# Optimization experiments

Measured on AMD Instinct MI355X. Metric: run time of the kernel, lower is better.

## Reference

```python
import jax, jax.numpy as jnp
import numpy as np

N = 131072  # time steps
D = 4       # SDE state dimension


def setup_inputs() -> dict:
    key = jax.random.key(0)
    k = jax.random.split(key, 6)
    F = 0.1 * jax.random.normal(k[0], (D, D), jnp.float32)  # only shape/dtype used by filter
    H = jnp.zeros((1, D), jnp.float32).at[0, 0].set(1.0)    # observe first state component
    P_inf = jnp.eye(D, dtype=jnp.float32)
    # stable per-step transitions: spectral radius ~0.9
    A_seq = 0.9 * jnp.eye(D, dtype=jnp.float32)[None] + 0.02 * jax.random.normal(k[1], (N, D, D), jnp.float32)
    # PSD process noise per step
    S = 0.05 * jax.random.normal(k[2], (N, D, D), jnp.float32)
    Q_seq = jnp.einsum('nij,nkj->nik', S, S) + 1e-3 * jnp.eye(D, dtype=jnp.float32)[None]
    residual = jax.random.normal(k[3], (N,), jnp.float32)   # y - mean_fn(times)
    mask = jnp.ones((N,), jnp.float32)                      # all steps observed
    R_seq = 0.1 + 0.05 * jax.random.uniform(k[4], (N,), jnp.float32)  # noise_var + floor
    return dict(F=F, H=H, P_inf=P_inf, A_seq=A_seq, Q_seq=Q_seq,
                residual=residual, mask=mask, R_seq=R_seq)


def _kalman_filter(F, H, P_inf, A_seq, Q_seq, residual, mask, R_seq):
    d = F.shape[0]
    eye = jnp.eye(d, dtype=F.dtype)
    h = H[0]  # (d,)
    log_2pi = jnp.log(2.0 * jnp.pi).astype(F.dtype)

    def step(carry, inputs):
        m, P = carry
        A, Q, r_n, mask_n, R_n = inputs
        m_pred = A @ m
        P_pred = A @ P @ A.T + Q
        P_pred = 0.5 * (P_pred + P_pred.T)
        Ph = P_pred @ h                 # (d,)
        S = h @ Ph + R_n                # innovation variance
        innov = r_n - h @ m_pred
        is_obs = mask_n == 1
        S_safe = jnp.where(is_obs, S, 1.0)
        K = jnp.where(is_obs, Ph / S_safe, jnp.zeros_like(Ph))
        m_new = m_pred + K * innov
        I_KH = eye - K[:, None] * h[None, :]
        P_new = I_KH @ P_pred @ I_KH.T + R_n * (K[:, None] * K[None, :])
        P_new = 0.5 * (P_new + P_new.T)
        ll = jnp.where(is_obs, -0.5 * (log_2pi + jnp.log(S_safe) + innov * innov / S_safe), 0.0)
        return (m_new, P_new), (m_pred, P_pred, m_new, P_new, ll)

    m0 = jnp.zeros(d, dtype=F.dtype)
    _, (m_pred_seq, P_pred_seq, m_filt_seq, P_filt_seq, ll_seq) = jax.lax.scan(
        step, (m0, P_inf), (A_seq, Q_seq, residual, mask, R_seq))
    return m_pred_seq, P_pred_seq, m_filt_seq, P_filt_seq, jnp.sum(ll_seq)


def _rts_smoother(m_pred_seq, P_pred_seq, m_filt_seq, P_filt_seq, A_seq):
    def step(carry, inputs):
        m_ns, P_ns = carry
        m_f, P_f, m_pn, P_pn, A_n = inputs
        J = jnp.linalg.solve(P_pn.T, A_n @ P_f.T).T
        m_s = m_f + J @ (m_ns - m_pn)
        P_s = P_f + J @ (P_ns - P_pn) @ J.T
        P_s = 0.5 * (P_s + P_s.T)
        return (m_s, P_s), (m_s, P_s)

    m_T = m_filt_seq[-1]
    P_T = P_filt_seq[-1]
    inputs = (m_filt_seq[:-1], P_filt_seq[:-1], m_pred_seq[1:], P_pred_seq[1:], A_seq[1:])
    _, (m_s, P_s) = jax.lax.scan(step, (m_T, P_T), inputs, reverse=True)
    return (jnp.concatenate([m_s, m_T[None]], axis=0),
            jnp.concatenate([P_s, P_T[None]], axis=0))


def reference(F, H, P_inf, A_seq, Q_seq, residual, mask, R_seq):
    m_pred, P_pred, m_filt, P_filt, log_marginal = _kalman_filter(
        F, H, P_inf, A_seq, Q_seq, residual, mask, R_seq)
    m_smooth, P_smooth = _rts_smoother(m_pred, P_pred, m_filt, P_filt, A_seq)
    h = H[0]
    means = m_smooth @ h                                   # (N,) observation-space means
    vars_ = jnp.einsum('i,nij,j->n', h, P_smooth, h)       # (N,) marginal variances
    return means, vars_, log_marginal
```

## Files before the change

### kernel.cpp

```cpp
#include <hip/hip_runtime.h>
#include <math.h>

#define NN 131072
#define WUP 32
#define TPB 256
#define NBLK (NN / TPB)
#define WINF (TPB + WUP + 1)
#define WINB (TPB + WUP - 1)
#define LOG2PI 1.8378770664093453f

typedef __attribute__((ext_vector_type(2))) float f2;

__device__ float4 g_f[5][NN];
__device__ float4 g_J[4][NN];
__device__ float4 g_W0[NN];
__device__ float4 g_W1[NN];
__device__ float2 g_W2[NN];
__device__ float4 g_u[NN];
__device__ double g_llb[NBLK];

__device__ __forceinline__ f2 bc(float s) {
  f2 r = {s, s};
  return r;
}
#define PF(a, b, c) __builtin_elementwise_fma((a), (b), (c))

template <int E>
__device__ __forceinline__ void ldpk(const float4 (*s)[E], int w, f2* M) {
#pragma unroll
  for (int c = 0; c < 4; ++c) {
    float4 v = s[c][w];
    M[2 * c] = f2{v.x, v.y};
    M[2 * c + 1] = f2{v.z, v.w};
  }
}

__device__ __forceinline__ void sym_rows(const float4 t0, const float4 t1, const float2 t2,
                                         f2* M) {
  M[0] = f2{t0.x, t0.y};
  M[1] = f2{t0.z, t0.w};
  M[2] = f2{t0.y, t1.x};
  M[3] = f2{t1.y, t1.z};
  M[4] = f2{t0.z, t1.y};
  M[5] = f2{t1.w, t2.x};
  M[6] = f2{t0.w, t1.z};
  M[7] = f2{t2.x, t2.y};
}

__device__ __forceinline__ void kf_step_pk(const f2* __restrict__ AT, const f2* __restrict__ Q,
                                           float r, float mk, float R, f2* __restrict__ m,
                                           f2* __restrict__ P, float& Ss, float& innov,
                                           bool& obs) {
  float m0 = m[0][0], m1 = m[0][1], m2_ = m[1][0], m3 = m[1][1];
  f2 mp[2];
#pragma unroll
  for (int p = 0; p < 2; ++p) {
    f2 acc = AT[p] * bc(m0);
    acc = PF(bc(m1), AT[2 + p], acc);
    acc = PF(bc(m2_), AT[4 + p], acc);
    acc = PF(bc(m3), AT[6 + p], acc);
    mp[p] = acc;
  }

  f2 T[8];
#pragma unroll
  for (int i = 0; i < 4; ++i) {
    float a0 = AT[0 + (i >> 1)][i & 1];
    float a1 = AT[2 + (i >> 1)][i & 1];
    float a2 = AT[4 + (i >> 1)][i & 1];
    float a3 = AT[6 + (i >> 1)][i & 1];
#pragma unroll
    for (int p = 0; p < 2; ++p) {
      f2 acc = P[p] * bc(a0);
      acc = PF(bc(a1), P[2 + p], acc);
      acc = PF(bc(a2), P[4 + p], acc);
      acc = PF(bc(a3), P[6 + p], acc);
      T[2 * i + p] = acc;
    }
  }

  f2 Pp[8];
#pragma unroll
  for (int i = 0; i < 4; ++i) {
    float t0 = T[2 * i][0], t1 = T[2 * i][1], t2 = T[2 * i + 1][0], t3 = T[2 * i + 1][1];
#pragma unroll
    for (int p = 0; p < 2; ++p) {
      f2 acc = PF(bc(t0), AT[p], Q[2 * i + p]);
      acc = PF(bc(t1), AT[2 + p], acc);
      acc = PF(bc(t2), AT[4 + p], acc);
      acc = PF(bc(t3), AT[6 + p], acc);
      Pp[2 * i + p] = acc;
    }
  }

  float S = Pp[0][0] + R;
  innov = r - mp[0][0];
  obs = (mk == 1.0f);
  Ss = obs ? S : 1.0f;
  float kf = obs ? __builtin_amdgcn_rcpf(S) : 0.0f;
  f2 K[2] = {Pp[0] * bc(kf), Pp[1] * bc(kf)};
#pragma unroll
  for (int p = 0; p < 2; ++p) m[p] = PF(K[p], bc(innov), mp[p]);

#pragma unroll
  for (int i = 0; i < 4; ++i) {
    float Ki = K[i >> 1][i & 1];
#pragma unroll
    for (int p = 0; p < 2; ++p) P[2 * i + p] = PF(bc(-Ki), Pp[p], Pp[2 * i + p]);
  }
}

__device__ __forceinline__ void chol_solve_pk(const f2* __restrict__ S, const f2* __restrict__ T,
                                              f2* __restrict__ X) {
  float s00 = S[0][0];
  float s10 = S[2][0], s11 = S[2][1];
  float s20 = S[4][0], s21 = S[4][1], s22 = S[5][0];
  float s30 = S[6][0], s31 = S[6][1], s32 = S[7][0], s33 = S[7][1];
  float i00 = __builtin_amdgcn_rsqf(s00);
  float l10 = s10 * i00, l20 = s20 * i00, l30 = s30 * i00;
  float i11 = __builtin_amdgcn_rsqf(s11 - l10 * l10);
  float l21 = (s21 - l20 * l10) * i11;
  float l31 = (s31 - l30 * l10) * i11;
  float i22 = __builtin_amdgcn_rsqf(s22 - l20 * l20 - l21 * l21);
  float l32 = (s32 - l30 * l20 - l31 * l21) * i22;
  float i33 = __builtin_amdgcn_rsqf(s33 - l30 * l30 - l31 * l31 - l32 * l32);
#pragma unroll
  for (int c = 0; c < 4; ++c) {
    float t0 = T[0 + (c >> 1)][c & 1];
    float t1 = T[2 + (c >> 1)][c & 1];
    float t2 = T[4 + (c >> 1)][c & 1];
    float t3 = T[6 + (c >> 1)][c & 1];
    float y0 = t0 * i00;
    float y1 = (t1 - l10 * y0) * i11;
    float y2 = (t2 - l20 * y0 - l21 * y1) * i22;
    float y3 = (t3 - l30 * y0 - l31 * y1 - l32 * y2) * i33;
    float x3 = y3 * i33;
    float x2 = (y2 - l32 * x3) * i22;
    float x1 = (y1 - l21 * x2 - l31 * x3) * i11;
    float x0 = (y0 - l10 * x1 - l20 * x2 - l30 * x3) * i00;
    X[0 + (c >> 1)][c & 1] = x0;
    X[2 + (c >> 1)][c & 1] = x1;
    X[4 + (c >> 1)][c & 1] = x2;
    X[6 + (c >> 1)][c & 1] = x3;
  }
}

__device__ __forceinline__ void make_record_pk(int n, const f2* __restrict__ m,
                                               const f2* __restrict__ P,
                                               const f2* __restrict__ AT,
                                               const f2* __restrict__ Q) {
  float m0 = m[0][0], m1 = m[0][1], m2_ = m[1][0], m3 = m[1][1];
  f2 pm[2];
#pragma unroll
  for (int p = 0; p < 2; ++p) {
    f2 acc = AT[p] * bc(m0);
    acc = PF(bc(m1), AT[2 + p], acc);
    acc = PF(bc(m2_), AT[4 + p], acc);
    acc = PF(bc(m3), AT[6 + p], acc);
    pm[p] = acc;
  }

  f2 T[8];
#pragma unroll
  for (int i = 0; i < 4; ++i) {
    float a0 = AT[0 + (i >> 1)][i & 1];
    float a1 = AT[2 + (i >> 1)][i & 1];
    float a2 = AT[4 + (i >> 1)][i & 1];
    float a3 = AT[6 + (i >> 1)][i & 1];
#pragma unroll
    for (int p = 0; p < 2; ++p) {
      f2 acc = P[p] * bc(a0);
      acc = PF(bc(a1), P[2 + p], acc);
      acc = PF(bc(a2), P[4 + p], acc);
      acc = PF(bc(a3), P[6 + p], acc);
      T[2 * i + p] = acc;
    }
  }

  f2 Ppn[8];
#pragma unroll
  for (int i = 0; i < 4; ++i) {
    float t0 = T[2 * i][0], t1 = T[2 * i][1], t2 = T[2 * i + 1][0], t3 = T[2 * i + 1][1];
#pragma unroll
    for (int p = 0; p < 2; ++p) {
      f2 acc = PF(bc(t0), AT[p], Q[2 * i + p]);
      acc = PF(bc(t1), AT[2 + p], acc);
      acc = PF(bc(t2), AT[4 + p], acc);
      acc = PF(bc(t3), AT[6 + p], acc);
      Ppn[2 * i + p] = acc;
    }
  }

  f2 X[8];
  chol_solve_pk(Ppn, T, X);

  float p0 = pm[0][0], p1 = pm[0][1], p2 = pm[1][0], p3 = pm[1][1];
  f2 u[2];
#pragma unroll
  for (int p = 0; p < 2; ++p) {
    f2 acc = X[p] * bc(p0);
    acc = PF(bc(p1), X[2 + p], acc);
    acc = PF(bc(p2), X[4 + p], acc);
    acc = PF(bc(p3), X[6 + p], acc);
    u[p] = m[p] - acc;
  }

  f2 Jp[8];
#pragma unroll
  for (int i = 0; i < 4; ++i) {
    float x0 = X[0 + (i >> 1)][i & 1];
    float x1 = X[2 + (i >> 1)][i & 1];
    float x2 = X[4 + (i >> 1)][i & 1];
    float x3 = X[6 + (i >> 1)][i & 1];
#pragma unroll
    for (int p = 0; p < 2; ++p) {
      f2 acc = Ppn[p] * bc(x0);
      acc = PF(bc(x1), Ppn[2 + p], acc);
      acc = PF(bc(x2), Ppn[4 + p], acc);
      acc = PF(bc(x3), Ppn[6 + p], acc);
      Jp[2 * i + p] = acc;
    }
  }
  f2 W[8];
#pragma unroll
  for (int i = 0; i < 4; ++i) {
    float j0 = Jp[2 * i][0], j1 = Jp[2 * i][1], j2 = Jp[2 * i + 1][0], j3 = Jp[2 * i + 1][1];
#pragma unroll
    for (int p = 0; p < 2; ++p) {
      f2 acc = X[p] * bc(j0);
      acc = PF(bc(j1), X[2 + p], acc);
      acc = PF(bc(j2), X[4 + p], acc);
      acc = PF(bc(j3), X[6 + p], acc);
      W[2 * i + p] = P[2 * i + p] - acc;
    }
  }

#pragma unroll
  for (int i = 0; i < 4; ++i)
    g_J[i][n] = make_float4(X[2 * i][0], X[2 * i][1], X[2 * i + 1][0], X[2 * i + 1][1]);
  g_W0[n] = make_float4(W[0][0], W[0][1], W[1][0], W[1][1]);
  g_W1[n] = make_float4(W[2][1], W[3][0], W[3][1], W[5][0]);
  g_W2[n] = make_float2(W[5][1], W[7][1]);
  g_u[n] = make_float4(u[0][0], u[0][1], u[1][0], u[1][1]);
}

__device__ __forceinline__ void rts_affine_pk(const f2* __restrict__ X, const f2* __restrict__ W,
                                              const f2* __restrict__ u, f2* __restrict__ ms,
                                              f2* __restrict__ Ps) {
  float s0 = ms[0][0], s1 = ms[0][1], s2 = ms[1][0], s3 = ms[1][1];
  f2 nms[2];
#pragma unroll
  for (int p = 0; p < 2; ++p) {
    f2 acc = PF(bc(s0), X[p], u[p]);
    acc = PF(bc(s1), X[2 + p], acc);
    acc = PF(bc(s2), X[4 + p], acc);
    acc = PF(bc(s3), X[6 + p], acc);
    nms[p] = acc;
  }
  f2 V[8];
#pragma unroll
  for (int i = 0; i < 4; ++i) {
    float x0 = X[0 + (i >> 1)][i & 1];
    float x1 = X[2 + (i >> 1)][i & 1];
    float x2 = X[4 + (i >> 1)][i & 1];
    float x3 = X[6 + (i >> 1)][i & 1];
#pragma unroll
    for (int p = 0; p < 2; ++p) {
      f2 acc = Ps[p] * bc(x0);
      acc = PF(bc(x1), Ps[2 + p], acc);
      acc = PF(bc(x2), Ps[4 + p], acc);
      acc = PF(bc(x3), Ps[6 + p], acc);
      V[2 * i + p] = acc;
    }
  }
#pragma unroll
  for (int i = 0; i < 4; ++i) {
    float v0 = V[2 * i][0], v1 = V[2 * i][1], v2 = V[2 * i + 1][0], v3 = V[2 * i + 1][1];
#pragma unroll
    for (int p = 0; p < 2; ++p) {
      f2 acc = PF(bc(v0), X[p], W[2 * i + p]);
      acc = PF(bc(v1), X[2 + p], acc);
      acc = PF(bc(v2), X[4 + p], acc);
      acc = PF(bc(v3), X[6 + p], acc);
      Ps[2 * i + p] = acc;
    }
  }
  ms[0] = nms[0];
  ms[1] = nms[1];
}

__global__ __launch_bounds__(TPB, 1) void fwd_kernel(const float* __restrict__ P_inf,
                                                     const float* __restrict__ A_seq,
                                                     const float* __restrict__ Q_seq,
                                                     const float* __restrict__ residual,
                                                     const float* __restrict__ mask,
                                                     const float* __restrict__ R_seq) {
  __shared__ float4 sAT[4][WINF];
  __shared__ float4 sQ0[WINF], sQ1[WINF];
  __shared__ float2 sQ2[WINF];
  __shared__ float4 sRM[WINF];
  __shared__ double sh[TPB];

  const int B = blockIdx.x * TPB;
  const int base = B - WUP;
  const float4* Af4 = (const float4*)A_seq;
  const float4* Qf4 = (const float4*)Q_seq;
  for (int f = threadIdx.x; f < WINF * 4; f += TPB) {
    int w = f >> 2, c = f & 3;
    int k = base + w;
    k = k < 0 ? 0 : (k > NN - 1 ? NN - 1 : k);
    float4 rowA = Af4[(size_t)k * 4 + c];
    ((float*)&sAT[0][w])[c] = rowA.x;
    ((float*)&sAT[1][w])[c] = rowA.y;
    ((float*)&sAT[2][w])[c] = rowA.z;
    ((float*)&sAT[3][w])[c] = rowA.w;
    float4 rowQ = Qf4[(size_t)k * 4 + c];
    if (c == 0) {
      sQ0[w] = rowQ;
    } else if (c == 1) {
      sQ1[w].x = rowQ.y;
      sQ1[w].y = rowQ.z;
      sQ1[w].z = rowQ.w;
    } else if (c == 2) {
      sQ1[w].w = rowQ.z;
      sQ2[w].x = rowQ.w;
    } else {
      sQ2[w].y = rowQ.w;
    }
  }
  for (int w = threadIdx.x; w < WINF; w += TPB) {
    int k = base + w;
    k = k < 0 ? 0 : (k > NN - 1 ? NN - 1 : k);
    sRM[w] = make_float4(residual[k], R_seq[k], mask[k], 0.f);
  }
  __syncthreads();

  const int t = threadIdx.x;
  const int n = B + t;
  int s0 = n - WUP;
  if (s0 < 0) s0 = 0;

  f2 m[2] = {f2{0.f, 0.f}, f2{0.f, 0.f}};
  f2 P[8];
#pragma unroll
  for (int i = 0; i < 4; ++i) {
    P[2 * i] = f2{P_inf[i * 4 + 0], P_inf[i * 4 + 1]};
    P[2 * i + 1] = f2{P_inf[i * 4 + 2], P_inf[i * 4 + 3]};
  }

  float Ss = 1.f, innov = 0.f;
  bool obs = false;
#pragma unroll 2
  for (int k = s0; k <= n; ++k) {
    int w = k - base;
    f2 AT[8], Q[8];
    ldpk<WINF>(sAT, w, AT);
    sym_rows(sQ0[w], sQ1[w], sQ2[w], Q);
    float4 rm = sRM[w];
    kf_step_pk(AT, Q, rm.x, rm.z, rm.y, m, P, Ss, innov, obs);
  }

#pragma unroll
  for (int c = 0; c < 4; ++c)
    g_f[c][n] = make_float4(P[2 * c][0], P[2 * c][1], P[2 * c + 1][0], P[2 * c + 1][1]);
  g_f[4][n] = make_float4(m[0][0], m[0][1], m[1][0], m[1][1]);

  if (n < NN - 1) {
    int w = n + 1 - base;
    f2 AT[8], Q[8];
    ldpk<WINF>(sAT, w, AT);
    sym_rows(sQ0[w], sQ1[w], sQ2[w], Q);
    make_record_pk(n, m, P, AT, Q);
  }

  sh[t] = obs ? (double)(-0.5f * (LOG2PI + logf(Ss) + innov * innov / Ss)) : 0.0;
  __syncthreads();
#pragma unroll
  for (int w = TPB / 2; w > 0; w >>= 1) {
    if (t < w) sh[t] += sh[t + w];
    __syncthreads();
  }
  if (t == 0) g_llb[blockIdx.x] = sh[0];
}

__global__ __launch_bounds__(TPB, 1) void bwd_kernel(float* __restrict__ out) {
  __shared__ float4 sX[4][WINB];
  __shared__ float4 sW0[WINB], sW1[WINB];
  __shared__ float2 sW2[WINB];
  __shared__ float4 su[WINB];
  __shared__ double shd[TPB];

  const int B = blockIdx.x * TPB;
  const int t = threadIdx.x;
  const int n = B + t;
  int e = n + WUP;
  if (e > NN - 1) e = NN - 1;

  f2 ms[2], Ps[8];
#pragma unroll
  for (int c = 0; c < 4; ++c) {
    float4 v = g_f[c][e];
    Ps[2 * c] = f2{v.x, v.y};
    Ps[2 * c + 1] = f2{v.z, v.w};
  }
  {
    float4 v = g_f[4][e];
    ms[0] = f2{v.x, v.y};
    ms[1] = f2{v.z, v.w};
  }

  for (int f = t; f < WINB * 4; f += TPB) {
    int w = f >> 2, c = f & 3;
    int k = B + w;
    if (k > NN - 1) k = NN - 1;
    sX[c][w] = g_J[c][k];
  }
  for (int w = t; w < WINB; w += TPB) {
    int k = B + w;
    if (k > NN - 1) k = NN - 1;
    sW0[w] = g_W0[k];
    sW1[w] = g_W1[k];
    sW2[w] = g_W2[k];
    su[w] = g_u[k];
  }
  __syncthreads();

#pragma unroll 2
  for (int k = e - 1; k >= n; --k) {
    int w = k - B;
    f2 X[8], W[8];
    ldpk<WINB>(sX, w, X);
    sym_rows(sW0[w], sW1[w], sW2[w], W);
    float4 v = su[w];
    f2 u[2] = {f2{v.x, v.y}, f2{v.z, v.w}};
    rts_affine_pk(X, W, u, ms, Ps);
  }

  out[n] = ms[0][0];
  out[NN + n] = Ps[0][0];

  if (blockIdx.x == 0) {
    double acc = 0.0;
    for (int i = t; i < NBLK; i += TPB) acc += g_llb[i];
    shd[t] = acc;
    __syncthreads();
#pragma unroll
    for (int w = TPB / 2; w > 0; w >>= 1) {
      if (t < w) shd[t] += shd[t + w];
      __syncthreads();
    }
    if (t == 0) out[2 * NN] = (float)shd[0];
  }
}

extern "C" void kernel_launch(void* const* d_in, const int* in_sizes, int n_in, void* d_out,
                              int out_size, void* d_ws, size_t ws_size, hipStream_t stream) {
  const float* P_inf = (const float*)d_in[2];
  const float* A_seq = (const float*)d_in[3];
  const float* Q_seq = (const float*)d_in[4];
  const float* residual = (const float*)d_in[5];
  const float* mask = (const float*)d_in[6];
  const float* R_seq = (const float*)d_in[7];
  float* out = (float*)d_out;

  fwd_kernel<<<NBLK, TPB, 0, stream>>>(P_inf, A_seq, Q_seq, residual, mask, R_seq);
  bwd_kernel<<<NBLK, TPB, 0, stream>>>(out);
}
```

Baseline: 119.0 us.

## Replace serial windowed RTS backward recursion with parallel associative scan

The backward kernel previously had each thread serially apply up to WUP affine RTS steps from a warm-up window. It now composes those affine maps (J, W, u) with a log-depth Hillis-Steele scan in shared memory over 288 elements, using 320-thread blocks, and then applies the composed map to the boundary smoothed state. This cuts the per-thread dependent chain from about 32 steps to about 9 scan levels. In exchange it needs more arithmetic per level (a full matrix compose), two barriers per level, and extra shared-memory traffic.

```diff
diff --git a/kernel.cpp b/kernel.cpp
--- a/kernel.cpp
+++ b/kernel.cpp
@@ -6,7 +6,8 @@
 #define TPB 256
 #define NBLK (NN / TPB)
 #define WINF (TPB + WUP + 1)
-#define WINB (TPB + WUP - 1)
+#define BTPB 320
+#define SCAN_N (TPB + WUP)
 #define LOG2PI 1.8378770664093453f
 
 typedef __attribute__((ext_vector_type(2))) float f2;
@@ -242,51 +243,6 @@
   g_W1[n] = make_float4(W[2][1], W[3][0], W[3][1], W[5][0]);
   g_W2[n] = make_float2(W[5][1], W[7][1]);
   g_u[n] = make_float4(u[0][0], u[0][1], u[1][0], u[1][1]);
-}
-
-__device__ __forceinline__ void rts_affine_pk(const f2* __restrict__ X, const f2* __restrict__ W,
-                                              const f2* __restrict__ u, f2* __restrict__ ms,
-                                              f2* __restrict__ Ps) {
-  float s0 = ms[0][0], s1 = ms[0][1], s2 = ms[1][0], s3 = ms[1][1];
-  f2 nms[2];
-#pragma unroll
-  for (int p = 0; p < 2; ++p) {
-    f2 acc = PF(bc(s0), X[p], u[p]);
-    acc = PF(bc(s1), X[2 + p], acc);
-    acc = PF(bc(s2), X[4 + p], acc);
-    acc = PF(bc(s3), X[6 + p], acc);
-    nms[p] = acc;
-  }
-  f2 V[8];
-#pragma unroll
-  for (int i = 0; i < 4; ++i) {
-    float x0 = X[0 + (i >> 1)][i & 1];
-    float x1 = X[2 + (i >> 1)][i & 1];
-    float x2 = X[4 + (i >> 1)][i & 1];
-    float x3 = X[6 + (i >> 1)][i & 1];
-#pragma unroll
-    for (int p = 0; p < 2; ++p) {
-      f2 acc = Ps[p] * bc(x0);
-      acc = PF(bc(x1), Ps[2 + p], acc);
-      acc = PF(bc(x2), Ps[4 + p], acc);
-      acc = PF(bc(x3), Ps[6 + p], acc);
-      V[2 * i + p] = acc;
-    }
-  }
-#pragma unroll
-  for (int i = 0; i < 4; ++i) {
-    float v0 = V[2 * i][0], v1 = V[2 * i][1], v2 = V[2 * i + 1][0], v3 = V[2 * i + 1][1];
-#pragma unroll
-    for (int p = 0; p < 2; ++p) {
-      f2 acc = PF(bc(v0), X[p], W[2 * i + p]);
-      acc = PF(bc(v1), X[2 + p], acc);
-      acc = PF(bc(v2), X[4 + p], acc);
-      acc = PF(bc(v3), X[6 + p], acc);
-      Ps[2 * i + p] = acc;
-    }
-  }
-  ms[0] = nms[0];
-  ms[1] = nms[1];
 }
 
 __global__ __launch_bounds__(TPB, 1) void fwd_kernel(const float* __restrict__ P_inf,
@@ -383,66 +339,163 @@
   if (t == 0) g_llb[blockIdx.x] = sh[0];
 }
 
-__global__ __launch_bounds__(TPB, 1) void bwd_kernel(float* __restrict__ out) {
-  __shared__ float4 sX[4][WINB];
-  __shared__ float4 sW0[WINB], sW1[WINB];
-  __shared__ float2 sW2[WINB];
-  __shared__ float4 su[WINB];
+__global__ __launch_bounds__(BTPB, 1) void bwd_kernel(float* __restrict__ out) {
+  __shared__ float4 pJ[4][SCAN_N];
+  __shared__ float4 pW0[SCAN_N], pW1[SCAN_N];
+  __shared__ float2 pW2[SCAN_N];
+  __shared__ float4 pu[SCAN_N];
   __shared__ double shd[TPB];
 
   const int B = blockIdx.x * TPB;
   const int t = threadIdx.x;
-  const int n = B + t;
-  int e = n + WUP;
-  if (e > NN - 1) e = NN - 1;
-
-  f2 ms[2], Ps[8];
+  const bool own = (t < SCAN_N);
+  const int k = B + t;
+
+  const int ii = (B + SCAN_N <= NN - 1) ? (B + SCAN_N) : (NN - 1);
+  f2 Pi[8], mi[2];
 #pragma unroll
   for (int c = 0; c < 4; ++c) {
-    float4 v = g_f[c][e];
-    Ps[2 * c] = f2{v.x, v.y};
-    Ps[2 * c + 1] = f2{v.z, v.w};
+    float4 v = g_f[c][ii];
+    Pi[2 * c] = f2{v.x, v.y};
+    Pi[2 * c + 1] = f2{v.z, v.w};
   }
   {
-    float4 v = g_f[4][e];
-    ms[0] = f2{v.x, v.y};
-    ms[1] = f2{v.z, v.w};
-  }
-
-  for (int f = t; f < WINB * 4; f += TPB) {
-    int w = f >> 2, c = f & 3;
-    int k = B + w;
-    if (k > NN - 1) k = NN - 1;
-    sX[c][w] = g_J[c][k];
-  }
-  for (int w = t; w < WINB; w += TPB) {
-    int k = B + w;
-    if (k > NN - 1) k = NN - 1;
-    sW0[w] = g_W0[k];
-    sW1[w] = g_W1[k];
-    sW2[w] = g_W2[k];
-    su[w] = g_u[k];
-  }
-  __syncthreads();
-
-#pragma unroll 2
-  for (int k = e - 1; k >= n; --k) {
-    int w = k - B;
-    f2 X[8], W[8];
-    ldpk<WINB>(sX, w, X);
-    sym_rows(sW0[w], sW1[w], sW2[w], W);
-    float4 v = su[w];
-    f2 u[2] = {f2{v.x, v.y}, f2{v.z, v.w}};
-    rts_affine_pk(X, W, u, ms, Ps);
-  }
-
-  out[n] = ms[0][0];
-  out[NN + n] = Ps[0][0];
+    float4 v = g_f[4][ii];
+    mi[0] = f2{v.x, v.y};
+    mi[1] = f2{v.z, v.w};
+  }
+
+  f2 X[8], W[8], u[2];
+  if (own && k < NN - 1) {
+#pragma unroll
+    for (int c = 0; c < 4; ++c) {
+      float4 v = g_J[c][k];
+      X[2 * c] = f2{v.x, v.y};
+      X[2 * c + 1] = f2{v.z, v.w};
+    }
+    sym_rows(g_W0[k], g_W1[k], g_W2[k], W);
+    float4 v = g_u[k];
+    u[0] = f2{v.x, v.y};
+    u[1] = f2{v.z, v.w};
+  } else {
+    X[0] = f2{1.f, 0.f}; X[1] = f2{0.f, 0.f};
+    X[2] = f2{0.f, 1.f}; X[3] = f2{0.f, 0.f};
+    X[4] = f2{0.f, 0.f}; X[5] = f2{1.f, 0.f};
+    X[6] = f2{0.f, 0.f}; X[7] = f2{0.f, 1.f};
+#pragma unroll
+    for (int i = 0; i < 8; ++i) W[i] = f2{0.f, 0.f};
+    u[0] = f2{0.f, 0.f};
+    u[1] = f2{0.f, 0.f};
+  }
+
+  for (int d = 1; d < SCAN_N; d <<= 1) {
+    if (own) {
+#pragma unroll
+      for (int c = 0; c < 4; ++c)
+        pJ[c][t] = make_float4(X[2 * c][0], X[2 * c][1], X[2 * c + 1][0], X[2 * c + 1][1]);
+      pW0[t] = make_float4(W[0][0], W[0][1], W[1][0], W[1][1]);
+      pW1[t] = make_float4(W[2][1], W[3][0], W[3][1], W[5][0]);
+      pW2[t] = make_float2(W[5][1], W[7][1]);
+      pu[t] = make_float4(u[0][0], u[0][1], u[1][0], u[1][1]);
+    }
+    __syncthreads();
+    const bool act = own && (t + d < SCAN_N);
+    f2 Xb[8], Wb[8], ub[2];
+    if (act) {
+      const int s = t + d;
+#pragma unroll
+      for (int c = 0; c < 4; ++c) {
+        float4 v = pJ[c][s];
+        Xb[2 * c] = f2{v.x, v.y};
+        Xb[2 * c + 1] = f2{v.z, v.w};
+      }
+      sym_rows(pW0[s], pW1[s], pW2[s], Wb);
+      float4 v = pu[s];
+      ub[0] = f2{v.x, v.y};
+      ub[1] = f2{v.z, v.w};
+    }
+    __syncthreads();
+    if (act) {
+      f2 Xc[8];
+#pragma unroll
+      for (int i = 0; i < 4; ++i) {
+        float b0 = Xb[2 * i][0], b1 = Xb[2 * i][1], b2 = Xb[2 * i + 1][0], b3 = Xb[2 * i + 1][1];
+#pragma unroll
+        for (int p = 0; p < 2; ++p) {
+          f2 acc = X[p] * bc(b0);
+          acc = PF(bc(b1), X[2 + p], acc);
+          acc = PF(bc(b2), X[4 + p], acc);
+          acc = PF(bc(b3), X[6 + p], acc);
+          Xc[2 * i + p] = acc;
+        }
+      }
+      float ub0 = ub[0][0], ub1 = ub[0][1], ub2 = ub[1][0], ub3 = ub[1][1];
+      f2 uc[2];
+#pragma unroll
+      for (int p = 0; p < 2; ++p) {
+        f2 acc = PF(bc(ub0), X[p], u[p]);
+        acc = PF(bc(ub1), X[2 + p], acc);
+        acc = PF(bc(ub2), X[4 + p], acc);
+        acc = PF(bc(ub3), X[6 + p], acc);
+        uc[p] = acc;
+      }
+      f2 V[8];
+#pragma unroll
+      for (int q = 0; q < 4; ++q) {
+        float w0 = Wb[2 * q][0], w1 = Wb[2 * q][1], w2 = Wb[2 * q + 1][0], w3 = Wb[2 * q + 1][1];
+#pragma unroll
+        for (int p = 0; p < 2; ++p) {
+          f2 acc = X[p] * bc(w0);
+          acc = PF(bc(w1), X[2 + p], acc);
+          acc = PF(bc(w2), X[4 + p], acc);
+          acc = PF(bc(w3), X[6 + p], acc);
+          V[2 * q + p] = acc;
+        }
+      }
+      f2 Wc[8];
+#pragma unroll
+      for (int i = 0; i < 4; ++i) {
+        float x0 = X[0 + (i >> 1)][i & 1];
+        float x1 = X[2 + (i >> 1)][i & 1];
+        float x2 = X[4 + (i >> 1)][i & 1];
+        float x3 = X[6 + (i >> 1)][i & 1];
+#pragma unroll
+        for (int p = 0; p < 2; ++p) {
+          f2 acc = PF(bc(x0), V[p], W[2 * i + p]);
+          acc = PF(bc(x1), V[2 + p], acc);
+          acc = PF(bc(x2), V[4 + p], acc);
+          acc = PF(bc(x3), V[6 + p], acc);
+          Wc[2 * i + p] = acc;
+        }
+      }
+#pragma unroll
+      for (int i = 0; i < 8; ++i) {
+        X[i] = Xc[i];
+        W[i] = Wc[i];
+      }
+      u[0] = uc[0];
+      u[1] = uc[1];
+    }
+  }
+
+  if (t < TPB) {
+    float x00 = X[0][0], x01 = X[2][0], x02 = X[4][0], x03 = X[6][0];
+    float mean = u[0][0] + x00 * mi[0][0] + x01 * mi[0][1] + x02 * mi[1][0] + x03 * mi[1][1];
+    float t0 = Pi[0][0] * x00 + Pi[0][1] * x01 + Pi[1][0] * x02 + Pi[1][1] * x03;
+    float t1 = Pi[2][0] * x00 + Pi[2][1] * x01 + Pi[3][0] * x02 + Pi[3][1] * x03;
+    float t2 = Pi[4][0] * x00 + Pi[4][1] * x01 + Pi[5][0] * x02 + Pi[5][1] * x03;
+    float t3 = Pi[6][0] * x00 + Pi[6][1] * x01 + Pi[7][0] * x02 + Pi[7][1] * x03;
+    float var = W[0][0] + x00 * t0 + x01 * t1 + x02 * t2 + x03 * t3;
+    out[B + t] = mean;
+    out[NN + B + t] = var;
+  }
 
   if (blockIdx.x == 0) {
-    double acc = 0.0;
-    for (int i = t; i < NBLK; i += TPB) acc += g_llb[i];
-    shd[t] = acc;
+    if (t < TPB) {
+      double acc = 0.0;
+      for (int i = t; i < NBLK; i += TPB) acc += g_llb[i];
+      shd[t] = acc;
+    }
     __syncthreads();
 #pragma unroll
     for (int w = TPB / 2; w > 0; w >>= 1) {
@@ -464,5 +517,5 @@
   float* out = (float*)d_out;
 
   fwd_kernel<<<NBLK, TPB, 0, stream>>>(P_inf, A_seq, Q_seq, residual, mask, R_seq);
-  bwd_kernel<<<NBLK, TPB, 0, stream>>>(out);
-}
+  bwd_kernel<<<NBLK, BTPB, 0, stream>>>(out);
+}
```

Result: faster. 114.3 us (-4.0%).

## Replace backward RTS matrix recursion with forward row-vector propagation of h

Applied to the files above, without the earlier changes.

Since only h·m and h·P·h are needed, the backward smoother now propagates a row vector r = h·J_n·J_{n+1}… forward through the warmup window, accumulating scalar contributions from the affine offsets u and W. This replaces per-step 4x4 matrix-matrix products (P' = J P Jᵀ + W) with vector-matrix products and quadratic forms, which cuts arithmetic per step substantially. J is stored transposed to suit the new access pattern. Numerical behaviour changes in summation order.

```diff
diff --git a/kernel.cpp b/kernel.cpp
--- a/kernel.cpp
+++ b/kernel.cpp
@@ -237,56 +237,12 @@
 
 #pragma unroll
   for (int i = 0; i < 4; ++i)
-    g_J[i][n] = make_float4(X[2 * i][0], X[2 * i][1], X[2 * i + 1][0], X[2 * i + 1][1]);
+    g_J[i][n] = make_float4(X[0 + (i >> 1)][i & 1], X[2 + (i >> 1)][i & 1],
+                            X[4 + (i >> 1)][i & 1], X[6 + (i >> 1)][i & 1]);
   g_W0[n] = make_float4(W[0][0], W[0][1], W[1][0], W[1][1]);
   g_W1[n] = make_float4(W[2][1], W[3][0], W[3][1], W[5][0]);
   g_W2[n] = make_float2(W[5][1], W[7][1]);
   g_u[n] = make_float4(u[0][0], u[0][1], u[1][0], u[1][1]);
-}
-
-__device__ __forceinline__ void rts_affine_pk(const f2* __restrict__ X, const f2* __restrict__ W,
-                                              const f2* __restrict__ u, f2* __restrict__ ms,
-                                              f2* __restrict__ Ps) {
-  float s0 = ms[0][0], s1 = ms[0][1], s2 = ms[1][0], s3 = ms[1][1];
-  f2 nms[2];
-#pragma unroll
-  for (int p = 0; p < 2; ++p) {
-    f2 acc = PF(bc(s0), X[p], u[p]);
-    acc = PF(bc(s1), X[2 + p], acc);
-    acc = PF(bc(s2), X[4 + p], acc);
-    acc = PF(bc(s3), X[6 + p], acc);
-    nms[p] = acc;
-  }
-  f2 V[8];
-#pragma unroll
-  for (int i = 0; i < 4; ++i) {
-    float x0 = X[0 + (i >> 1)][i & 1];
-    float x1 = X[2 + (i >> 1)][i & 1];
-    float x2 = X[4 + (i >> 1)][i & 1];
-    float x3 = X[6 + (i >> 1)][i & 1];
-#pragma unroll
-    for (int p = 0; p < 2; ++p) {
-      f2 acc = Ps[p] * bc(x0);
-      acc = PF(bc(x1), Ps[2 + p], acc);
-      acc = PF(bc(x2), Ps[4 + p], acc);
-      acc = PF(bc(x3), Ps[6 + p], acc);
-      V[2 * i + p] = acc;
-    }
-  }
-#pragma unroll
-  for (int i = 0; i < 4; ++i) {
-    float v0 = V[2 * i][0], v1 = V[2 * i][1], v2 = V[2 * i + 1][0], v3 = V[2 * i + 1][1];
-#pragma unroll
-    for (int p = 0; p < 2; ++p) {
-      f2 acc = PF(bc(v0), X[p], W[2 * i + p]);
-      acc = PF(bc(v1), X[2 + p], acc);
-      acc = PF(bc(v2), X[4 + p], acc);
-      acc = PF(bc(v3), X[6 + p], acc);
-      Ps[2 * i + p] = acc;
-    }
-  }
-  ms[0] = nms[0];
-  ms[1] = nms[1];
 }
 
 __global__ __launch_bounds__(TPB, 1) void fwd_kernel(const float* __restrict__ P_inf,
@@ -384,7 +340,7 @@
 }
 
 __global__ __launch_bounds__(TPB, 1) void bwd_kernel(float* __restrict__ out) {
-  __shared__ float4 sX[4][WINB];
+  __shared__ float4 sJ[4][WINB];
   __shared__ float4 sW0[WINB], sW1[WINB];
   __shared__ float2 sW2[WINB];
   __shared__ float4 su[WINB];
@@ -396,24 +352,24 @@
   int e = n + WUP;
   if (e > NN - 1) e = NN - 1;
 
-  f2 ms[2], Ps[8];
+  f2 Pi[8], mi[2];
 #pragma unroll
   for (int c = 0; c < 4; ++c) {
     float4 v = g_f[c][e];
-    Ps[2 * c] = f2{v.x, v.y};
-    Ps[2 * c + 1] = f2{v.z, v.w};
+    Pi[2 * c] = f2{v.x, v.y};
+    Pi[2 * c + 1] = f2{v.z, v.w};
   }
   {
     float4 v = g_f[4][e];
-    ms[0] = f2{v.x, v.y};
-    ms[1] = f2{v.z, v.w};
+    mi[0] = f2{v.x, v.y};
+    mi[1] = f2{v.z, v.w};
   }
 
   for (int f = t; f < WINB * 4; f += TPB) {
     int w = f >> 2, c = f & 3;
     int k = B + w;
     if (k > NN - 1) k = NN - 1;
-    sX[c][w] = g_J[c][k];
+    sJ[c][w] = g_J[c][k];
   }
   for (int w = t; w < WINB; w += TPB) {
     int k = B + w;
@@ -425,19 +381,58 @@
   }
   __syncthreads();
 
+  f2 r01 = f2{1.f, 0.f}, r23 = f2{0.f, 0.f};
+  float alpha = 0.f, omega = 0.f;
 #pragma unroll 2
-  for (int k = e - 1; k >= n; --k) {
+  for (int k = n; k < e; ++k) {
     int w = k - B;
-    f2 X[8], W[8];
-    ldpk<WINB>(sX, w, X);
+    float4 j0 = sJ[0][w], j1 = sJ[1][w], j2 = sJ[2][w], j3 = sJ[3][w];
+    f2 W[8];
     sym_rows(sW0[w], sW1[w], sW2[w], W);
-    float4 v = su[w];
-    f2 u[2] = {f2{v.x, v.y}, f2{v.z, v.w}};
-    rts_affine_pk(X, W, u, ms, Ps);
-  }
-
-  out[n] = ms[0][0];
-  out[NN + n] = Ps[0][0];
+    float4 uv = su[w];
+    float r0 = r01[0], r1 = r01[1], r2 = r23[0], r3 = r23[1];
+    alpha += r0 * uv.x + r1 * uv.y + r2 * uv.z + r3 * uv.w;
+    f2 s01 = W[0] * bc(r0);
+    s01 = PF(bc(r1), W[2], s01);
+    s01 = PF(bc(r2), W[4], s01);
+    s01 = PF(bc(r3), W[6], s01);
+    f2 s23 = W[1] * bc(r0);
+    s23 = PF(bc(r1), W[3], s23);
+    s23 = PF(bc(r2), W[5], s23);
+    s23 = PF(bc(r3), W[7], s23);
+    f2 os = r01 * s01;
+    os = PF(r23, s23, os);
+    omega += os[0] + os[1];
+    f2 ja = f2{j0.x, j0.y}, jb = f2{j1.x, j1.y}, jc = f2{j2.x, j2.y}, jd = f2{j3.x, j3.y};
+    f2 je = f2{j0.z, j0.w}, jf = f2{j1.z, j1.w}, jg = f2{j2.z, j2.w}, jh = f2{j3.z, j3.w};
+    f2 n01 = ja * bc(r0);
+    n01 = PF(bc(r1), jb, n01);
+    n01 = PF(bc(r2), jc, n01);
+    n01 = PF(bc(r3), jd, n01);
+    f2 n23 = je * bc(r0);
+    n23 = PF(bc(r1), jf, n23);
+    n23 = PF(bc(r2), jg, n23);
+    n23 = PF(bc(r3), jh, n23);
+    r01 = n01;
+    r23 = n23;
+  }
+
+  {
+    float r0 = r01[0], r1 = r01[1], r2 = r23[0], r3 = r23[1];
+    float mean = alpha + r0 * mi[0][0] + r1 * mi[0][1] + r2 * mi[1][0] + r3 * mi[1][1];
+    f2 s01 = Pi[0] * bc(r0);
+    s01 = PF(bc(r1), Pi[2], s01);
+    s01 = PF(bc(r2), Pi[4], s01);
+    s01 = PF(bc(r3), Pi[6], s01);
+    f2 s23 = Pi[1] * bc(r0);
+    s23 = PF(bc(r1), Pi[3], s23);
+    s23 = PF(bc(r2), Pi[5], s23);
+    s23 = PF(bc(r3), Pi[7], s23);
+    f2 vs = r01 * s01;
+    vs = PF(r23, s23, vs);
+    out[n] = mean;
+    out[NN + n] = omega + vs[0] + vs[1];
+  }
 
   if (blockIdx.x == 0) {
     double acc = 0.0;
```

Result: faster. 115.8 us (-2.7%).
